# Kernel optimization log

Hardware: AMD Instinct MI355X
Metric: run time of the kernel (lower is better)

Reference implementation:

```python
import jax, jax.numpy as jnp
import numpy as np

B, C, H, W = 16, 256, 64, 64
DA = 64  # attention_size


def setup_inputs() -> dict:
    key = jax.random.key(0)
    ks = jax.random.split(key, 7)
    s_in = 1.0 / np.sqrt(C)
    return {
        "x": jax.random.normal(ks[0], (B, C, H, W), jnp.float32),
        "Wq": jax.random.normal(ks[1], (DA, C), jnp.float32) * s_in,
        "bq": jax.random.normal(ks[2], (DA,), jnp.float32) * 0.01,
        "Wk": jax.random.normal(ks[3], (DA, C), jnp.float32) * s_in,
        "bk": jax.random.normal(ks[4], (DA,), jnp.float32) * 0.01,
        "Wv": jax.random.normal(ks[5], (C, C), jnp.float32) * s_in,
        "bv": jax.random.normal(ks[6], (C,), jnp.float32) * 0.01,
    }


def reference(x, Wq, bq, Wk, bk, Wv, bv):
    b, c, h, w = x.shape
    n = h * w
    xf = x.reshape(b, c, n)                      # [B,C,N]
    q = jnp.einsum('ac,bcn->ban', Wq, xf) + bq[None, :, None]   # [B,DA,N]
    k = jnp.einsum('ac,bcn->ban', Wk, xf) + bk[None, :, None]   # [B,DA,N]
    v = jnp.einsum('dc,bcn->bdn', Wv, xf) + bv[None, :, None]   # [B,C,N]
    # scores[b,i,j] = q[:,i] . k[:,j], scaled by 1/sqrt(H*W) (as in source)
    scores = jnp.einsum('bai,baj->bij', q, k) / jnp.sqrt(jnp.float32(n))
    attn = jax.nn.softmax(scores, axis=-1)       # [B,N,N]
    out = jnp.einsum('bcj,bij->bci', v, attn)    # [B,C,N]
    return out.reshape(b, c, h, w) + x
```

## Files before the change

### kernel.cpp

```cpp
#include <hip/hip_runtime.h>
#include <hip/hip_bf16.h>
#include <stdint.h>


#define B_  16
#define C_  256
#define N_  4096
#define DA_ 64
#define MSHIFT 2.0f

typedef __attribute__((ext_vector_type(8))) short short8;
typedef __attribute__((ext_vector_type(4))) float f32x4;

__device__ int g_isf32;

__device__ __forceinline__ short f2bf(float f) {
    union { float f; uint32_t u; } v; v.f = f;
    uint32_t r = v.u + 0x7fffu + ((v.u >> 16) & 1u);
    return (short)(r >> 16);
}
__device__ __forceinline__ float bf2f(uint16_t s) {
    union { uint32_t u; float f; } v; v.u = ((uint32_t)s) << 16;
    return v.f;
}
__device__ __forceinline__ uint32_t pkbf(float a, float b) {
    union { __hip_bfloat162 h; uint32_t u; } c;
    c.h = __float22bfloat162_rn(make_float2(a, b));
    return c.u;
}

__device__ __forceinline__ void gld_lds16(const uint16_t* g, uint16_t* l) {
    __builtin_amdgcn_global_load_lds(
        (const __attribute__((address_space(1))) unsigned int*)g,
        (__attribute__((address_space(3))) unsigned int*)l,
        16, 0, 0);
}

__global__ void detect_kernel(const void* __restrict__ x) {
    const uint16_t* p = (const uint16_t*)x;
    int i = threadIdx.x;
    uint16_t u = p[2 * i];
    int e = (u >> 7) & 0xFF;
    unsigned long long m = __ballot(e >= 112 && e <= 132);
    if (i == 0) g_isf32 = (__popcll(m) < 32) ? 1 : 0;
}

template<bool F32>
__device__ __forceinline__ void proj_body(
    const void* __restrict__ xv,
    const void* __restrict__ Wqv, const void* __restrict__ bqv,
    const void* __restrict__ Wkv, const void* __restrict__ bkv,
    const void* __restrict__ Wvv, const void* __restrict__ bvv,
    uint16_t* __restrict__ Q, uint16_t* __restrict__ K, uint16_t* __restrict__ Vt,
    float* bias_lds, uint16_t* buf)
{
    const int tid = threadIdx.x;
    const int b  = blockIdx.x >> 6;
    const int n0 = (blockIdx.x & 63) * 64;
    const int w = tid >> 6, lane = tid & 63, q = lane >> 4, ln = lane & 15;

    for (int idx = tid; idx < 384; idx += 256) {
        float bias;
        if (F32) {
            bias = (idx < 64)  ? ((const float*)bqv)[idx]
                 : (idx < 128) ? ((const float*)bkv)[idx - 64]
                               : ((const float*)bvv)[idx - 128];
        } else {
            bias = (idx < 64)  ? bf2f(((const uint16_t*)bqv)[idx])
                 : (idx < 128) ? bf2f(((const uint16_t*)bkv)[idx - 64])
                               : bf2f(((const uint16_t*)bvv)[idx - 128]);
        }
        bias_lds[idx] = bias;
    }

    {
        int cbase = tid >> 2, s0 = tid & 3;
        #pragma unroll
        for (int cc = 0; cc < 4; cc++) {
            int c = cc * 64 + cbase;
            if (F32) {
                const float* xr = (const float*)xv + ((size_t)b * C_ + c) * N_ + n0;
                #pragma unroll
                for (int k = 0; k < 4; k++) {
                    int nl = (s0 + 4 * k) * 4;
                    float4 v = *(const float4*)(xr + nl);
                    buf[(nl + 0) * 264 + c] = (uint16_t)f2bf(v.x);
                    buf[(nl + 1) * 264 + c] = (uint16_t)f2bf(v.y);
                    buf[(nl + 2) * 264 + c] = (uint16_t)f2bf(v.z);
                    buf[(nl + 3) * 264 + c] = (uint16_t)f2bf(v.w);
                }
            } else {
                const uint16_t* xr = (const uint16_t*)xv + ((size_t)b * C_ + c) * N_ + n0;
                #pragma unroll
                for (int k = 0; k < 2; k++) {
                    int nl = s0 * 16 + k * 8;
                    short8 v = *(const short8*)(xr + nl);
                    #pragma unroll
                    for (int e = 0; e < 8; e++)
                        buf[(nl + e) * 264 + c] = (uint16_t)v[e];
                }
            }
        }
    }
    __syncthreads();

    f32x4 acc[6][4];
    #pragma unroll
    for (int mt = 0; mt < 6; mt++)
        #pragma unroll
        for (int nt = 0; nt < 4; nt++) acc[mt][nt] = (f32x4)0.0f;

    for (int kc = 0; kc < 8; kc++) {
        short8 af[6];
        #pragma unroll
        for (int mt = 0; mt < 6; mt++) {
            int row = (w * 6 + mt) * 16 + ln;
            if (F32) {
                const float* src = (row < 64) ? (const float*)Wqv + (size_t)row * 256
                                 : (row < 128) ? (const float*)Wkv + (size_t)(row - 64) * 256
                                               : (const float*)Wvv + (size_t)(row - 128) * 256;
                float4 a0 = *(const float4*)(src + kc * 32 + q * 8);
                float4 a1 = *(const float4*)(src + kc * 32 + q * 8 + 4);
                union { short8 s; uint32_t u[4]; } c;
                c.u[0] = pkbf(a0.x, a0.y); c.u[1] = pkbf(a0.z, a0.w);
                c.u[2] = pkbf(a1.x, a1.y); c.u[3] = pkbf(a1.z, a1.w);
                af[mt] = c.s;
            } else {
                const uint16_t* src = (row < 64) ? (const uint16_t*)Wqv + (size_t)row * 256
                                    : (row < 128) ? (const uint16_t*)Wkv + (size_t)(row - 64) * 256
                                                  : (const uint16_t*)Wvv + (size_t)(row - 128) * 256;
                af[mt] = *(const short8*)(src + kc * 32 + q * 8);
            }
        }
        short8 bfr[4];
        #pragma unroll
        for (int nt = 0; nt < 4; nt++)
            bfr[nt] = *(const short8*)&buf[(nt * 16 + ln) * 264 + kc * 32 + q * 8];
        #pragma unroll
        for (int mt = 0; mt < 6; mt++)
            #pragma unroll
            for (int nt = 0; nt < 4; nt++)
                acc[mt][nt] = __builtin_amdgcn_mfma_f32_16x16x32_bf16(
                    af[mt], bfr[nt], acc[mt][nt], 0, 0, 0);
    }
    __syncthreads();

    #pragma unroll
    for (int mt = 0; mt < 6; mt++) {
        int rowb = (w * 6 + mt) * 16 + q * 4;
        #pragma unroll
        for (int r = 0; r < 4; r++) {
            float bias = bias_lds[rowb + r];
            #pragma unroll
            for (int nt = 0; nt < 4; nt++)
                buf[(rowb + r) * 72 + nt * 16 + ln] =
                    (uint16_t)f2bf(acc[mt][nt][r] + bias);
        }
    }
    __syncthreads();

    {
        int a = tid & 63, nb = tid >> 6;
        uint16_t* Qb = Q + ((size_t)b * N_ + n0) * 64;
        uint16_t* Kb = K + ((size_t)b * N_ + n0) * 64;
        #pragma unroll 4
        for (int j = 0; j < 16; j++) {
            int n = nb + 4 * j;
            Qb[(size_t)n * 64 + a] = buf[a * 72 + n];
            Kb[(size_t)n * 64 + a] = buf[(64 + a) * 72 + n];
        }
    }
    {
        int ch = tid & 7;
        #pragma unroll
        for (int p = 0; p < 8; p++) {
            int c = p * 32 + (tid >> 3);
            short8 v = *(const short8*)&buf[(128 + c) * 72 + ch * 8];
            *(short8*)(Vt + ((size_t)b * C_ + c) * N_ + n0 + ch * 8) = v;
        }
    }
}

__global__ __launch_bounds__(256, 2) void proj_kernel(
    const void* xv, const void* Wqv, const void* bqv, const void* Wkv,
    const void* bkv, const void* Wvv, const void* bvv,
    uint16_t* Q, uint16_t* K, uint16_t* Vt)
{
    __shared__ float    bias_lds[384];
    __shared__ uint16_t buf[384 * 72];
    if (g_isf32) proj_body<true >(xv, Wqv, bqv, Wkv, bkv, Wvv, bvv, Q, K, Vt, bias_lds, buf);
    else         proj_body<false>(xv, Wqv, bqv, Wkv, bkv, Wvv, bvv, Q, K, Vt, bias_lds, buf);
}

template<bool F32>
__device__ __forceinline__ void flash_body(
    const uint16_t* __restrict__ Q, const uint16_t* __restrict__ K,
    const uint16_t* __restrict__ Vt, const void* __restrict__ xv,
    void* __restrict__ outv,
    uint16_t* Klds2, uint16_t* Plds, float* l_lds)
{
    const int tid = threadIdx.x;
    const int b  = blockIdx.x >> 5;
    const int i0 = (blockIdx.x & 31) * 128;
    const int w = tid >> 6, lane = tid & 63, q = lane >> 4, ln = lane & 15;
    const int rw = w >> 2, cw = w & 3;

    const float c1 = 1.4426950408889634f / 64.0f;

    short8 qf[2];
    {
        const uint16_t* qrow = Q + ((size_t)b * N_ + (i0 + w * 16 + ln)) * 64;
        qf[0] = *(const short8*)(qrow + q * 8);
        qf[1] = *(const short8*)(qrow + 32 + q * 8);
    }

    const uint16_t* Kb = K + (size_t)b * N_ * 64;
    const uint16_t* vrow[4];
    #pragma unroll
    for (int ct = 0; ct < 4; ct++)
        vrow[ct] = Vt + ((size_t)b * C_ + (cw * 64 + ct * 16 + ln)) * N_ + q * 8;

    const int krow = lane >> 3, kslot = lane & 7;
    const size_t kgoff = (size_t)(w * 8 + krow) * 64 + (size_t)((kslot ^ krow) * 8);
    uint16_t* kdst0 = Klds2 + (w << 9);

    const int kb0 = ln * 64 + ((q ^ (ln & 7)) * 8);
    const int kb1 = ln * 64 + (((4 + q) ^ (ln & 7)) * 8);

    float l_run = 0.0f;
    f32x4 O[4][4];
    #pragma unroll
    for (int rg = 0; rg < 4; rg++)
        #pragma unroll
        for (int ct = 0; ct < 4; ct++) O[rg][ct] = (f32x4)0.0f;

    gld_lds16(Kb + kgoff, kdst0);
    __syncthreads();

    for (int it = 0; it < 64; it++) {
        const int j0 = it * 64;
        const int par = it & 1;

        if (it < 63)
            gld_lds16(Kb + (size_t)(j0 + 64) * 64 + kgoff,
                      Klds2 + ((par ^ 1) << 12) + (w << 9));

        const uint16_t* Kt = Klds2 + (par << 12);

        f32x4 s[4];
        #pragma unroll
        for (int jt = 0; jt < 4; jt++) s[jt] = (f32x4)0.0f;

        __builtin_amdgcn_s_setprio(1);
        #pragma unroll
        for (int jt = 0; jt < 4; jt++) {
            short8 kf0 = *(const short8*)(Kt + jt * 1024 + kb0);
            s[jt] = __builtin_amdgcn_mfma_f32_16x16x32_bf16(kf0, qf[0], s[jt], 0, 0, 0);
            short8 kf1 = *(const short8*)(Kt + jt * 1024 + kb1);
            s[jt] = __builtin_amdgcn_mfma_f32_16x16x32_bf16(kf1, qf[1], s[jt], 0, 0, 0);
        }
        __builtin_amdgcn_s_setprio(0);

        uint16_t* prow = &Plds[(w * 16 + ln) * 72 + q * 4];
        #pragma unroll
        for (int jt = 0; jt < 4; jt++) {
            float p0 = exp2f(s[jt][0] * c1 - MSHIFT);
            float p1 = exp2f(s[jt][1] * c1 - MSHIFT);
            float p2 = exp2f(s[jt][2] * c1 - MSHIFT);
            float p3 = exp2f(s[jt][3] * c1 - MSHIFT);
            l_run += (p0 + p1) + (p2 + p3);
            uint2 pk; pk.x = pkbf(p0, p1); pk.y = pkbf(p2, p3);
            *(uint2*)&prow[jt * 16] = pk;
        }
        __syncthreads();

        __builtin_amdgcn_s_setprio(1);
        #pragma unroll
        for (int kst = 0; kst < 2; kst++) {
            short8 bfr[4];
            #pragma unroll
            for (int ct = 0; ct < 4; ct++)
                bfr[ct] = *(const short8*)(vrow[ct] + j0 + kst * 32);
            short8 af[4];
            #pragma unroll
            for (int rg = 0; rg < 4; rg++)
                af[rg] = *(const short8*)&Plds[(rw * 64 + rg * 16 + ln) * 72 + kst * 32 + q * 8];
            #pragma unroll
            for (int rg = 0; rg < 4; rg++)
                #pragma unroll
                for (int ct = 0; ct < 4; ct++)
                    O[rg][ct] = __builtin_amdgcn_mfma_f32_16x16x32_bf16(
                        af[rg], bfr[ct], O[rg][ct], 0, 0, 0);
        }
        __builtin_amdgcn_s_setprio(0);

        asm volatile("s_waitcnt vmcnt(0)" ::: "memory");
        __syncthreads();
    }

    l_run += __shfl_xor(l_run, 16);
    l_run += __shfl_xor(l_run, 32);
    if (lane < 16) l_lds[w * 16 + lane] = l_run;
    __syncthreads();

    #pragma unroll
    for (int rg = 0; rg < 4; rg++) {
        f32x4 lv = *(const f32x4*)&l_lds[rw * 64 + rg * 16 + q * 4];
        f32x4 li; li[0] = 1.0f/lv[0]; li[1] = 1.0f/lv[1]; li[2] = 1.0f/lv[2]; li[3] = 1.0f/lv[3];
        #pragma unroll
        for (int ct = 0; ct < 4; ct++) {
            int c = cw * 64 + ct * 16 + ln;
            size_t off = (size_t)c * N_ + i0 + rw * 64 + rg * 16 + q * 4;
            if (F32) {
                const float* xb = (const float*)xv + (size_t)b * C_ * N_;
                float* ob = (float*)outv + (size_t)b * C_ * N_;
                float4 xv4 = *(const float4*)(xb + off);
                float4 res;
                res.x = O[rg][ct][0] * li[0] + xv4.x;
                res.y = O[rg][ct][1] * li[1] + xv4.y;
                res.z = O[rg][ct][2] * li[2] + xv4.z;
                res.w = O[rg][ct][3] * li[3] + xv4.w;
                *(float4*)(ob + off) = res;
            } else {
                const uint16_t* xb = (const uint16_t*)xv + (size_t)b * C_ * N_;
                uint16_t* ob = (uint16_t*)outv + (size_t)b * C_ * N_;
                uint2 xp = *(const uint2*)(xb + off);
                uint2 res;
                res.x = pkbf(O[rg][ct][0] * li[0] + bf2f((uint16_t)(xp.x & 0xFFFF)),
                             O[rg][ct][1] * li[1] + bf2f((uint16_t)(xp.x >> 16)));
                res.y = pkbf(O[rg][ct][2] * li[2] + bf2f((uint16_t)(xp.y & 0xFFFF)),
                             O[rg][ct][3] * li[3] + bf2f((uint16_t)(xp.y >> 16)));
                *(uint2*)(ob + off) = res;
            }
        }
    }
}

__global__ __launch_bounds__(512, 4) void flash_kernel(
    const uint16_t* Q, const uint16_t* K, const uint16_t* Vt,
    const void* xv, void* outv)
{
    __shared__ uint16_t Klds2[2 * 64 * 64];
    __shared__ uint16_t Plds[128 * 72];
    __shared__ __align__(16) float l_lds[128];
    if (g_isf32) flash_body<true >(Q, K, Vt, xv, outv, Klds2, Plds, l_lds);
    else         flash_body<false>(Q, K, Vt, xv, outv, Klds2, Plds, l_lds);
}

extern "C" void kernel_launch(void* const* d_in, const int* in_sizes, int n_in,
                              void* d_out, int out_size, void* d_ws, size_t ws_size,
                              hipStream_t stream) {
    const void* x  = d_in[0];
    const void* Wq = d_in[1];
    const void* bq = d_in[2];
    const void* Wk = d_in[3];
    const void* bk = d_in[4];
    const void* Wv = d_in[5];
    const void* bv = d_in[6];

    uint16_t* Qw = (uint16_t*)d_ws;
    uint16_t* Kw = Qw + (size_t)B_ * N_ * DA_;
    uint16_t* Vw = Kw + (size_t)B_ * N_ * DA_;

    detect_kernel<<<dim3(1), dim3(64), 0, stream>>>(x);
    proj_kernel<<<dim3(B_ * 64), dim3(256), 0, stream>>>(x, Wq, bq, Wk, bk, Wv, bv, Qw, Kw, Vw);
    flash_kernel<<<dim3(B_ * 32), dim3(512), 0, stream>>>(Qw, Kw, Vw, x, d_out);
}
```

Measured before the change: 522.4 us.

## Triple-buffer K and double-buffer P to use one barrier per iteration

The flash loop now keeps three K tiles in LDS and prefetches two tiles ahead. It also alternates between two P buffers, so each iteration needs only one barrier, placed after a partial vmcnt wait, instead of two. The s_setprio hints around the MFMA sections are removed. The aim is to cut barrier stalls and hide global-load latency. The cost is that LDS per block grows from about 34KB to about 60KB, which may stop four 512-thread blocks from fitting on a CU and lower occupancy.

```diff
diff --git a/kernel.cpp b/kernel.cpp
--- a/kernel.cpp
+++ b/kernel.cpp
@@ -197,7 +197,7 @@
     const uint16_t* __restrict__ Q, const uint16_t* __restrict__ K,
     const uint16_t* __restrict__ Vt, const void* __restrict__ xv,
     void* __restrict__ outv,
-    uint16_t* Klds2, uint16_t* Plds, float* l_lds)
+    uint16_t* Klds3, uint16_t* Plds2, float* l_lds)
 {
     const int tid = threadIdx.x;
     const int b  = blockIdx.x >> 5;
@@ -222,7 +222,7 @@
 
     const int krow = lane >> 3, kslot = lane & 7;
     const size_t kgoff = (size_t)(w * 8 + krow) * 64 + (size_t)((kslot ^ krow) * 8);
-    uint16_t* kdst0 = Klds2 + (w << 9);
+    const int ldst = (w << 9);
 
     const int kb0 = ln * 64 + ((q ^ (ln & 7)) * 8);
     const int kb1 = ln * 64 + (((4 + q) ^ (ln & 7)) * 8);
@@ -234,24 +234,27 @@
         #pragma unroll
         for (int ct = 0; ct < 4; ct++) O[rg][ct] = (f32x4)0.0f;
 
-    gld_lds16(Kb + kgoff, kdst0);
-    __syncthreads();
+    gld_lds16(Kb + kgoff,        Klds3 + ldst);
+    gld_lds16(Kb + 4096 + kgoff, Klds3 + 4096 + ldst);
+    asm volatile("s_waitcnt vmcnt(1)" ::: "memory");
+    __builtin_amdgcn_s_barrier();
+
+    const uint16_t* kpre = Kb + 2 * 4096 + kgoff;
+    int bcur = 0, bnx2 = 2;
 
     for (int it = 0; it < 64; it++) {
         const int j0 = it * 64;
-        const int par = it & 1;
-
-        if (it < 63)
-            gld_lds16(Kb + (size_t)(j0 + 64) * 64 + kgoff,
-                      Klds2 + ((par ^ 1) << 12) + (w << 9));
-
-        const uint16_t* Kt = Klds2 + (par << 12);
+
+        if (it < 62) {
+            gld_lds16(kpre, Klds3 + bnx2 * 4096 + ldst);
+            kpre += 4096;
+        }
+
+        const uint16_t* Kt = Klds3 + bcur * 4096;
 
         f32x4 s[4];
         #pragma unroll
         for (int jt = 0; jt < 4; jt++) s[jt] = (f32x4)0.0f;
-
-        __builtin_amdgcn_s_setprio(1);
         #pragma unroll
         for (int jt = 0; jt < 4; jt++) {
             short8 kf0 = *(const short8*)(Kt + jt * 1024 + kb0);
@@ -259,9 +262,9 @@
             short8 kf1 = *(const short8*)(Kt + jt * 1024 + kb1);
             s[jt] = __builtin_amdgcn_mfma_f32_16x16x32_bf16(kf1, qf[1], s[jt], 0, 0, 0);
         }
-        __builtin_amdgcn_s_setprio(0);
-
-        uint16_t* prow = &Plds[(w * 16 + ln) * 72 + q * 4];
+
+        uint16_t* Pl = Plds2 + (it & 1) * 9216;
+        uint16_t* prow = &Pl[(w * 16 + ln) * 72 + q * 4];
         #pragma unroll
         for (int jt = 0; jt < 4; jt++) {
             float p0 = exp2f(s[jt][0] * c1 - MSHIFT);
@@ -272,9 +275,11 @@
             uint2 pk; pk.x = pkbf(p0, p1); pk.y = pkbf(p2, p3);
             *(uint2*)&prow[jt * 16] = pk;
         }
-        __syncthreads();
-
-        __builtin_amdgcn_s_setprio(1);
+
+        if (it < 62) asm volatile("s_waitcnt vmcnt(1) lgkmcnt(0)" ::: "memory");
+        else         asm volatile("s_waitcnt vmcnt(0) lgkmcnt(0)" ::: "memory");
+        __builtin_amdgcn_s_barrier();
+
         #pragma unroll
         for (int kst = 0; kst < 2; kst++) {
             short8 bfr[4];
@@ -284,7 +289,7 @@
             short8 af[4];
             #pragma unroll
             for (int rg = 0; rg < 4; rg++)
-                af[rg] = *(const short8*)&Plds[(rw * 64 + rg * 16 + ln) * 72 + kst * 32 + q * 8];
+                af[rg] = *(const short8*)&Pl[(rw * 64 + rg * 16 + ln) * 72 + kst * 32 + q * 8];
             #pragma unroll
             for (int rg = 0; rg < 4; rg++)
                 #pragma unroll
@@ -292,10 +297,9 @@
                     O[rg][ct] = __builtin_amdgcn_mfma_f32_16x16x32_bf16(
                         af[rg], bfr[ct], O[rg][ct], 0, 0, 0);
         }
-        __builtin_amdgcn_s_setprio(0);
-
-        asm volatile("s_waitcnt vmcnt(0)" ::: "memory");
-        __syncthreads();
+
+        bcur = (bcur == 2) ? 0 : bcur + 1;
+        bnx2 = (bnx2 == 2) ? 0 : bnx2 + 1;
     }
 
     l_run += __shfl_xor(l_run, 16);
@@ -340,11 +344,11 @@
     const uint16_t* Q, const uint16_t* K, const uint16_t* Vt,
     const void* xv, void* outv)
 {
-    __shared__ uint16_t Klds2[2 * 64 * 64];
-    __shared__ uint16_t Plds[128 * 72];
+    __shared__ uint16_t Klds3[3 * 64 * 64];
+    __shared__ uint16_t Plds2[2 * 128 * 72];
     __shared__ __align__(16) float l_lds[128];
-    if (g_isf32) flash_body<true >(Q, K, Vt, xv, outv, Klds2, Plds, l_lds);
-    else         flash_body<false>(Q, K, Vt, xv, outv, Klds2, Plds, l_lds);
+    if (g_isf32) flash_body<true >(Q, K, Vt, xv, outv, Klds3, Plds2, l_lds);
+    else         flash_body<false>(Q, K, Vt, xv, outv, Klds3, Plds2, l_lds);
 }
 
 extern "C" void kernel_launch(void* const* d_in, const int* in_sizes, int n_in,
```

Measured after the change: 523.2 us. Within noise of the previous version (+0.1%).
